# Kernel optimization log

Hardware: AMD Instinct MI355X
Metric: run time of the kernel (lower is better)

Reference implementation:

```python
import jax, jax.numpy as jnp
import numpy as np

N = 5_000_000   # hits
D = 6           # track-parameter dim (MSE sums over dim=1)
P = 50_000      # max particle_id (0 = noise)


def setup_inputs() -> dict:
    key = jax.random.key(0)
    ks = jax.random.split(key, 8)
    return {
        "W": jax.random.normal(ks[0], (N,), dtype=jnp.float32),
        "beta": jax.random.uniform(ks[1], (N,), dtype=jnp.float32, minval=1e-4, maxval=1.0 - 1e-4),
        "H": jax.random.normal(ks[2], (N, 8), dtype=jnp.float32),
        "pred": jax.random.normal(ks[3], (N, D), dtype=jnp.float32),
        "Y": jax.random.normal(ks[4], (N,), dtype=jnp.float32),
        "particle_id": jax.random.randint(ks[5], (N,), 0, P),
        "track_params": jax.random.normal(ks[6], (N, D), dtype=jnp.float32),
        "reconstructable": jax.random.randint(ks[7], (N,), 0, 2),
    }


def reference(W, beta, H, pred, Y, particle_id, track_params, reconstructable):
    # mask = reconstructable > 0 ; then object_loss on the masked subset.
    # Original loops over unique pids > 0; for each pid the contribution is
    # weight * sum(mse * M * pid) with weight = 1/sum(M * pid) == mean(mse over group).
    # Final: 100 * sum_over_groups(group_mean_mse) / num_groups.
    # We express it as one segment reduce over pid, weighting out
    # non-reconstructable hits and noise (pid == 0).
    mask = reconstructable > 0
    valid = mask & (particle_id > 0)
    w = valid.astype(pred.dtype)                                  # [N]
    mse = jnp.sum((pred - track_params) ** 2, axis=1)             # [N]
    sums = jax.ops.segment_sum(mse * w, particle_id, num_segments=P)   # [P]
    counts = jax.ops.segment_sum(w, particle_id, num_segments=P)       # [P]
    present = counts > 0
    means = jnp.where(present, sums / jnp.where(present, counts, 1.0), 0.0)
    K = jnp.sum(present).astype(pred.dtype)
    return 100.0 * jnp.sum(means) / K
```

## Files before the change

### kernel.cpp

```cpp
#include <hip/hip_runtime.h>

#define P_SEG 50000
#define PACK_C 16777216.0

__global__ __launch_bounds__(256) void
objloss_accum(const float* __restrict__ pred,
              const float* __restrict__ tp,
              const int* __restrict__ pid,
              const int* __restrict__ recon,
              double* __restrict__ bins,
              int n) {
    int i = blockIdx.x * blockDim.x + threadIdx.x;
    int base = i * 2;
    if (base >= n) return;

    if (base + 1 < n) {
        int2 pp = *reinterpret_cast<const int2*>(pid + base);
        int2 rr = *reinterpret_cast<const int2*>(recon + base);
        const float4* pa = reinterpret_cast<const float4*>(pred + (size_t)base * 6);
        const float4* tb = reinterpret_cast<const float4*>(tp   + (size_t)base * 6);
        float4 a0 = pa[0], a1 = pa[1], a2 = pa[2];
        float4 b0 = tb[0], b1 = tb[1], b2 = tb[2];

        float e0 = a0.x - b0.x, e1 = a0.y - b0.y, e2 = a0.z - b0.z;
        float e3 = a0.w - b0.w, e4 = a1.x - b1.x, e5 = a1.y - b1.y;
        float m0 = e0*e0 + e1*e1 + e2*e2 + e3*e3 + e4*e4 + e5*e5;

        float f0 = a1.z - b1.z, f1 = a1.w - b1.w, f2 = a2.x - b2.x;
        float f3 = a2.y - b2.y, f4 = a2.z - b2.z, f5 = a2.w - b2.w;
        float m1 = f0*f0 + f1*f1 + f2*f2 + f3*f3 + f4*f4 + f5*f5;

        bool v0 = (rr.x > 0) & (pp.x > 0) & (pp.x < P_SEG);
        bool v1 = (rr.y > 0) & (pp.y > 0) & (pp.y < P_SEG);
        if (v0) atomicAdd(&bins[pp.x], (double)m0 + PACK_C);
        if (v1) atomicAdd(&bins[pp.y], (double)m1 + PACK_C);
    } else {
        int p = pid[base];
        int r = recon[base];
        if ((r > 0) & (p > 0) & (p < P_SEG)) {
            float m = 0.0f;
            #pragma unroll
            for (int d = 0; d < 6; ++d) {
                float e = pred[(size_t)base * 6 + d] - tp[(size_t)base * 6 + d];
                m += e * e;
            }
            atomicAdd(&bins[p], (double)m + PACK_C);
        }
    }
}

__global__ __launch_bounds__(1024) void
objloss_finalize(const double* __restrict__ bins,
                 float* __restrict__ out) {
    __shared__ double s_sum[16];
    __shared__ double s_k[16];

    double local_sum = 0.0;
    double local_k = 0.0;
    for (int i = threadIdx.x; i < P_SEG; i += blockDim.x) {
        double v = bins[i];
        double cnt = floor(v * (1.0 / PACK_C));
        if (cnt > 0.0) {
            double s = v - cnt * PACK_C;
            local_sum += s / cnt;
            local_k += 1.0;
        }
    }
    #pragma unroll
    for (int off = 32; off > 0; off >>= 1) {
        local_sum += __shfl_down(local_sum, off);
        local_k   += __shfl_down(local_k, off);
    }
    int wave = threadIdx.x >> 6;
    int lane = threadIdx.x & 63;
    if (lane == 0) {
        s_sum[wave] = local_sum;
        s_k[wave] = local_k;
    }
    __syncthreads();
    if (threadIdx.x == 0) {
        double tot = 0.0, k = 0.0;
        #pragma unroll
        for (int w = 0; w < 16; ++w) {
            tot += s_sum[w];
            k += s_k[w];
        }
        out[0] = (k > 0.0) ? (float)(100.0 * tot / k) : 0.0f;
    }
}

extern "C" void kernel_launch(void* const* d_in, const int* in_sizes, int n_in,
                              void* d_out, int out_size, void* d_ws, size_t ws_size,
                              hipStream_t stream) {
    const float* pred  = (const float*)d_in[3];
    const int*   pid   = (const int*)  d_in[5];
    const float* tp    = (const float*)d_in[6];
    const int*   recon = (const int*)  d_in[7];
    int n = in_sizes[0];

    double* bins = (double*)d_ws;

    hipMemsetAsync(d_ws, 0, P_SEG * sizeof(double), stream);

    const int block = 256;
    int pairs = (n + 1) / 2;
    int grid = (pairs + block - 1) / block;
    objloss_accum<<<grid, block, 0, stream>>>(pred, tp, pid, recon, bins, n);
    objloss_finalize<<<1, 1024, 0, stream>>>(bins, (float*)d_out);
}
```

Measured before the change: 434.1 us.

## Privatize segment bins per XCD and use L2-scoped atomics with multi-block finalize

Gives each XCD its own copy of the per-particle bins, chosen from the hardware XCC id register, and issues non-system-scope global_atomic_add_f64 through inline asm. The aim is to keep atomic traffic inside each die's L2 instead of contending on one device-wide bin array across dies. The finalize becomes a two-stage reduction that sums the 8 copies across 256 blocks, then reduces the partials. The cost is 8x the memset and reduction work, and correctness depends on per-XCD L2 coherence being visible to the later kernels.

```diff
diff --git a/kernel.cpp b/kernel.cpp
--- a/kernel.cpp
+++ b/kernel.cpp
@@ -2,17 +2,28 @@
 
 #define P_SEG 50000
 #define PACK_C 16777216.0
+#define NBLK_FIN 256
+
+__device__ __forceinline__ int xcc_id() {
+    return __builtin_amdgcn_s_getreg(((4 - 1) << 11) | (0 << 6) | 20) & 7;
+}
+
+__device__ __forceinline__ void l2_atomic_add_f64(double* p, double v) {
+    asm volatile("global_atomic_add_f64 %0, %1, off" :: "v"(p), "v"(v) : "memory");
+}
 
 __global__ __launch_bounds__(256) void
-objloss_accum(const float* __restrict__ pred,
-              const float* __restrict__ tp,
-              const int* __restrict__ pid,
-              const int* __restrict__ recon,
-              double* __restrict__ bins,
-              int n) {
+objloss_accum_xcd(const float* __restrict__ pred,
+                  const float* __restrict__ tp,
+                  const int* __restrict__ pid,
+                  const int* __restrict__ recon,
+                  double* __restrict__ bins,
+                  int n) {
     int i = blockIdx.x * blockDim.x + threadIdx.x;
     int base = i * 2;
     if (base >= n) return;
+
+    double* mybins = bins + (size_t)xcc_id() * P_SEG;
 
     if (base + 1 < n) {
         int2 pp = *reinterpret_cast<const int2*>(pid + base);
@@ -30,10 +41,50 @@
         float f3 = a2.y - b2.y, f4 = a2.z - b2.z, f5 = a2.w - b2.w;
         float m1 = f0*f0 + f1*f1 + f2*f2 + f3*f3 + f4*f4 + f5*f5;
 
-        bool v0 = (rr.x > 0) & (pp.x > 0) & (pp.x < P_SEG);
-        bool v1 = (rr.y > 0) & (pp.y > 0) & (pp.y < P_SEG);
-        if (v0) atomicAdd(&bins[pp.x], (double)m0 + PACK_C);
-        if (v1) atomicAdd(&bins[pp.y], (double)m1 + PACK_C);
+        if ((rr.x > 0) & (pp.x > 0) & (pp.x < P_SEG))
+            l2_atomic_add_f64(&mybins[pp.x], (double)m0 + PACK_C);
+        if ((rr.y > 0) & (pp.y > 0) & (pp.y < P_SEG))
+            l2_atomic_add_f64(&mybins[pp.y], (double)m1 + PACK_C);
+    } else {
+        int p = pid[base];
+        int r = recon[base];
+        if ((r > 0) & (p > 0) & (p < P_SEG)) {
+            float m = 0.0f;
+            #pragma unroll
+            for (int d = 0; d < 6; ++d) {
+                float e = pred[(size_t)base * 6 + d] - tp[(size_t)base * 6 + d];
+                m += e * e;
+            }
+            l2_atomic_add_f64(&mybins[p], (double)m + PACK_C);
+        }
+    }
+}
+
+__global__ __launch_bounds__(256) void
+objloss_accum_dev(const float* __restrict__ pred,
+                  const float* __restrict__ tp,
+                  const int* __restrict__ pid,
+                  const int* __restrict__ recon,
+                  double* __restrict__ bins,
+                  int n) {
+    int i = blockIdx.x * blockDim.x + threadIdx.x;
+    int base = i * 2;
+    if (base >= n) return;
+    if (base + 1 < n) {
+        int2 pp = *reinterpret_cast<const int2*>(pid + base);
+        int2 rr = *reinterpret_cast<const int2*>(recon + base);
+        const float4* pa = reinterpret_cast<const float4*>(pred + (size_t)base * 6);
+        const float4* tb = reinterpret_cast<const float4*>(tp   + (size_t)base * 6);
+        float4 a0 = pa[0], a1 = pa[1], a2 = pa[2];
+        float4 b0 = tb[0], b1 = tb[1], b2 = tb[2];
+        float e0 = a0.x - b0.x, e1 = a0.y - b0.y, e2 = a0.z - b0.z;
+        float e3 = a0.w - b0.w, e4 = a1.x - b1.x, e5 = a1.y - b1.y;
+        float m0 = e0*e0 + e1*e1 + e2*e2 + e3*e3 + e4*e4 + e5*e5;
+        float f0 = a1.z - b1.z, f1 = a1.w - b1.w, f2 = a2.x - b2.x;
+        float f3 = a2.y - b2.y, f4 = a2.z - b2.z, f5 = a2.w - b2.w;
+        float m1 = f0*f0 + f1*f1 + f2*f2 + f3*f3 + f4*f4 + f5*f5;
+        if ((rr.x > 0) & (pp.x > 0) & (pp.x < P_SEG)) atomicAdd(&bins[pp.x], (double)m0 + PACK_C);
+        if ((rr.y > 0) & (pp.y > 0) & (pp.y < P_SEG)) atomicAdd(&bins[pp.y], (double)m1 + PACK_C);
     } else {
         int p = pid[base];
         int r = recon[base];
@@ -49,43 +100,57 @@
     }
 }
 
-__global__ __launch_bounds__(1024) void
-objloss_finalize(const double* __restrict__ bins,
-                 float* __restrict__ out) {
-    __shared__ double s_sum[16];
-    __shared__ double s_k[16];
-
-    double local_sum = 0.0;
-    double local_k = 0.0;
-    for (int i = threadIdx.x; i < P_SEG; i += blockDim.x) {
-        double v = bins[i];
+__global__ __launch_bounds__(256) void
+objloss_mid(const double* __restrict__ bins, int ncopies,
+            double* __restrict__ partials) {
+    double lsum = 0.0, lk = 0.0;
+    int stride = gridDim.x * blockDim.x;
+    for (int i = blockIdx.x * blockDim.x + threadIdx.x; i < P_SEG; i += stride) {
+        double v = 0.0;
+        for (int c = 0; c < ncopies; ++c) v += bins[(size_t)c * P_SEG + i];
         double cnt = floor(v * (1.0 / PACK_C));
         if (cnt > 0.0) {
-            double s = v - cnt * PACK_C;
-            local_sum += s / cnt;
-            local_k += 1.0;
+            lsum += (v - cnt * PACK_C) / cnt;
+            lk += 1.0;
         }
     }
     #pragma unroll
     for (int off = 32; off > 0; off >>= 1) {
-        local_sum += __shfl_down(local_sum, off);
-        local_k   += __shfl_down(local_k, off);
+        lsum += __shfl_down(lsum, off);
+        lk   += __shfl_down(lk, off);
     }
-    int wave = threadIdx.x >> 6;
-    int lane = threadIdx.x & 63;
-    if (lane == 0) {
-        s_sum[wave] = local_sum;
-        s_k[wave] = local_k;
-    }
+    __shared__ double ss[4], sk[4];
+    int w = threadIdx.x >> 6, lane = threadIdx.x & 63;
+    if (lane == 0) { ss[w] = lsum; sk[w] = lk; }
     __syncthreads();
     if (threadIdx.x == 0) {
-        double tot = 0.0, k = 0.0;
+        double t = 0.0, k = 0.0;
         #pragma unroll
-        for (int w = 0; w < 16; ++w) {
-            tot += s_sum[w];
-            k += s_k[w];
-        }
-        out[0] = (k > 0.0) ? (float)(100.0 * tot / k) : 0.0f;
+        for (int j = 0; j < 4; ++j) { t += ss[j]; k += sk[j]; }
+        partials[2 * blockIdx.x]     = t;
+        partials[2 * blockIdx.x + 1] = k;
+    }
+}
+
+__global__ __launch_bounds__(256) void
+objloss_final(const double* __restrict__ partials, float* __restrict__ out) {
+    int t = threadIdx.x;
+    double ls = 0.0, lk = 0.0;
+    if (t < NBLK_FIN) { ls = partials[2 * t]; lk = partials[2 * t + 1]; }
+    #pragma unroll
+    for (int off = 32; off > 0; off >>= 1) {
+        ls += __shfl_down(ls, off);
+        lk += __shfl_down(lk, off);
+    }
+    __shared__ double ss[4], sk[4];
+    int w = t >> 6, lane = t & 63;
+    if (lane == 0) { ss[w] = ls; sk[w] = lk; }
+    __syncthreads();
+    if (t == 0) {
+        double s = 0.0, k = 0.0;
+        #pragma unroll
+        for (int j = 0; j < 4; ++j) { s += ss[j]; k += sk[j]; }
+        out[0] = (k > 0.0) ? (float)(100.0 * s / k) : 0.0f;
     }
 }
 
@@ -98,13 +163,22 @@
     const int*   recon = (const int*)  d_in[7];
     int n = in_sizes[0];
 
-    double* bins = (double*)d_ws;
+    size_t need8 = (size_t)8 * P_SEG * sizeof(double) + 2 * NBLK_FIN * sizeof(double);
+    int ncopies = (ws_size >= need8) ? 8 : 1;
 
-    hipMemsetAsync(d_ws, 0, P_SEG * sizeof(double), stream);
+    double* bins     = (double*)d_ws;
+    double* partials = bins + (size_t)ncopies * P_SEG;
+
+    hipMemsetAsync(d_ws, 0, (size_t)ncopies * P_SEG * sizeof(double), stream);
 
     const int block = 256;
     int pairs = (n + 1) / 2;
     int grid = (pairs + block - 1) / block;
-    objloss_accum<<<grid, block, 0, stream>>>(pred, tp, pid, recon, bins, n);
-    objloss_finalize<<<1, 1024, 0, stream>>>(bins, (float*)d_out);
+    if (ncopies == 8)
+        objloss_accum_xcd<<<grid, block, 0, stream>>>(pred, tp, pid, recon, bins, n);
+    else
+        objloss_accum_dev<<<grid, block, 0, stream>>>(pred, tp, pid, recon, bins, n);
+
+    objloss_mid<<<NBLK_FIN, block, 0, stream>>>(bins, ncopies, partials);
+    objloss_final<<<1, block, 0, stream>>>(partials, (float*)d_out);
 }
```

After: 414.6 us. 1.05x faster.
